# Kernel tuning notes

Hardware: AMD Instinct MI355X
Metric: run time of the kernel (lower is better)

## Reference

```python
import jax, jax.numpy as jnp
import numpy as np

B, L, DIN, DH, DE = 16, 128, 768, 300, 100
ALPHA = 0.2
NEG = -9e15


def setup_inputs() -> dict:
    key = jax.random.key(0)
    k = jax.random.split(key, 7)
    s = lambda fan: 1.0 / np.sqrt(fan)
    return {
        "x": jax.random.normal(k[0], (B, L, DIN), jnp.float32),
        "adj": jax.random.randint(k[1], (B, L, L), 0, 2, jnp.int32),
        "edge_embedding": jax.random.normal(k[2], (B, L, L, DE), jnp.float32),
        "W": jax.random.normal(k[3], (DIN, DH), jnp.float32) * s(DIN),
        "a": jax.random.normal(k[4], (2 * DH, 1), jnp.float32) * s(2 * DH),
        "edge_map_w": jax.random.normal(k[5], (DH, DE), jnp.float32) * s(DE),
        "edge_map_b": jnp.zeros((DH,), jnp.float32),
        "edge_lin_w": jax.random.normal(k[6], (1, DH), jnp.float32) * s(DH),
        "edge_lin_b": jnp.zeros((1,), jnp.float32),
    }


def _forward(x, edge_embedding, W, a, edge_map_w, edge_map_b, edge_lin_w, edge_lin_b, adj):
    h = x @ W  # [B, L, DH]
    # Faithful to torch: h.repeat_interleave(L, dim=2).view(B, L*L, DH) scrambles
    # features: a_input_first[b, i*L+j, d] = h[b, i, (j*DH + d) // L].
    # So e1[b,i,j] = sum_d h[b,i,(j*DH+d)//L] * a[d] = h[b,i] . V[j], with V[j,k] =
    # sum of a[d] over d where (j*DH+d)//L == k. Build V once by scatter-add.
    idx = (jnp.arange(L)[:, None] * DH + jnp.arange(DH)[None, :]) // L  # [L, DH], values in [0, DH)
    a_first = a[:DH, 0]
    V = jnp.zeros((L, DH), h.dtype).at[jnp.arange(L)[:, None], idx].add(a_first[None, :])  # [L, DH]
    e1 = jnp.einsum('bik,jk->bij', h, V)  # [B, L, L]
    # Second half: h.repeat_interleave(L, dim=0).view(...) gives plain h_j tiling.
    e2 = h @ a[DH:, 0]  # [B, L], broadcast over i
    e = jax.nn.leaky_relu(e1 + e2[:, None, :], ALPHA)  # [B, L, L]
    # Edge-weight gate (use_edge_weight == 'yes'); note torch relu result is discarded.
    em = edge_embedding @ edge_map_w.T + edge_map_b  # [B, L, L, DH]
    ew = jax.nn.sigmoid(em @ edge_lin_w.T + edge_lin_b)[..., 0]  # [B, L, L]
    e_final = e * ew
    att = jax.nn.softmax(jnp.where(adj > 0, e_final, NEG), axis=2)  # dropout off (eval)
    return h + jnp.matmul(att, h)  # residual add, concat=False


def reference(x, adj, edge_embedding, W, a, edge_map_w, edge_map_b, edge_lin_w, edge_lin_b):
    return _forward(x, edge_embedding, W, a, edge_map_w, edge_map_b, edge_lin_w, edge_lin_b, adj)
```

## Files before the change

kernel.cpp:

```cpp
#include <hip/hip_runtime.h>
#include <hip/hip_bf16.h>


#define L 128
#define DH 300
#define DIN 768
#define DE 100
#define SPLITK 4
#define MROWS 2048
#define SL ((size_t)MROWS * DH)

typedef __bf16 bf16x8 __attribute__((ext_vector_type(8)));
typedef float f32x4 __attribute__((ext_vector_type(4)));
typedef unsigned short ushort_t;

__device__ __forceinline__ ushort_t f2bf(float f) {
    __bf16 h = (__bf16)f;
    ushort_t u;
    __builtin_memcpy(&u, &h, 2);
    return u;
}

__global__ __launch_bounds__(256) void k_small(
    const float* __restrict__ A,
    const float* __restrict__ EMW,
    const float* __restrict__ EMB,
    const float* __restrict__ ELW,
    const float* __restrict__ ELB,
    float* __restrict__ CV, float* __restrict__ C0,
    float* __restrict__ VW, int* __restrict__ VCOL)
{
    int t = threadIdx.x;
    if (blockIdx.x == 0) {
        if (t < DE) {
            float s = 0.f;
            for (int k = 0; k < DH; ++k)
                s += ELW[k] * EMW[k * DE + t];
            CV[t] = s;
        } else if (t == DE) {
            float s = 0.f;
            for (int k = 0; k < DH; ++k)
                s += ELW[k] * EMB[k];
            C0[0] = s + ELB[0];
        }
    } else {
        if (t < L) {
            int base = t * DH;
            int cm = base >> 7;
            float w0 = 0.f, w1 = 0.f, w2 = 0.f, w3 = 0.f;
            for (int j = 0; j < DH; ++j) {
                int u = ((base + j) >> 7) - cm;
                float av = A[j];
                w0 += (u == 0) ? av : 0.f;
                w1 += (u == 1) ? av : 0.f;
                w2 += (u == 2) ? av : 0.f;
                w3 += (u == 3) ? av : 0.f;
            }
            VCOL[t] = cm;
            VW[t * 4 + 0] = w0; VW[t * 4 + 1] = w1;
            VW[t * 4 + 2] = w2; VW[t * 4 + 3] = w3;
        }
    }
}

__global__ __launch_bounds__(256) void k_cvt(
    const float* __restrict__ Wm, ushort_t* __restrict__ WT)
{
    __shared__ float tile[64][65];
    int k0 = blockIdx.x * 64;
    int c0 = blockIdx.y * 64;
    int t = threadIdx.x;
#pragma unroll
    for (int s = 0; s < 16; ++s) {
        int idx = t + 256 * s;
        int kr = idx >> 6, cc = idx & 63;
        int c = c0 + cc;
        tile[kr][cc] = (c < DH) ? Wm[(size_t)(k0 + kr) * DH + c] : 0.f;
    }
    __syncthreads();
#pragma unroll
    for (int s = 0; s < 16; ++s) {
        int idx = t + 256 * s;
        int c = idx >> 6, kr = idx & 63;
        WT[(size_t)(c0 + c) * DIN + k0 + kr] = f2bf(tile[kr][c]);
    }
}

__global__ __launch_bounds__(256) void k_gemm(
    const float* __restrict__ X,
    const ushort_t* __restrict__ WT,
    float* __restrict__ HP)
{
    __shared__ ushort_t As[64 * 72];
    __shared__ ushort_t Bs[64 * 72];
    int t = threadIdx.x;
    int w = t >> 6;
    int lane = t & 63;
    int lr = lane & 15;
    int lk = lane >> 4;
    int r0 = blockIdx.y * 64;
    int c0 = blockIdx.x * 64;
    int kbase = blockIdx.z * (DIN / SPLITK);

    f32x4 acc[4];
#pragma unroll
    for (int ct = 0; ct < 4; ++ct) acc[ct] = (f32x4){0.f, 0.f, 0.f, 0.f};

    int srow = t >> 2, skq = (t & 3) * 16;

    for (int step = 0; step < 3; ++step) {
        int kk = kbase + step * 64;
        {
            const float4* xs = (const float4*)(X + (size_t)(r0 + srow) * DIN + kk + skq);
            float4 f0 = xs[0], f1 = xs[1], f2 = xs[2], f3 = xs[3];
            bf16x8 v0, v1;
            v0[0] = (__bf16)f0.x; v0[1] = (__bf16)f0.y; v0[2] = (__bf16)f0.z; v0[3] = (__bf16)f0.w;
            v0[4] = (__bf16)f1.x; v0[5] = (__bf16)f1.y; v0[6] = (__bf16)f1.z; v0[7] = (__bf16)f1.w;
            v1[0] = (__bf16)f2.x; v1[1] = (__bf16)f2.y; v1[2] = (__bf16)f2.z; v1[3] = (__bf16)f2.w;
            v1[4] = (__bf16)f3.x; v1[5] = (__bf16)f3.y; v1[6] = (__bf16)f3.z; v1[7] = (__bf16)f3.w;
            *(bf16x8*)&As[srow * 72 + skq] = v0;
            *(bf16x8*)&As[srow * 72 + skq + 8] = v1;
        }
        {
            const uint4* wp = (const uint4*)(WT + (size_t)(c0 + srow) * DIN + kk + skq);
            uint4 u0 = wp[0], u1 = wp[1];
            *(uint4*)&Bs[srow * 72 + skq] = u0;
            *(uint4*)&Bs[srow * 72 + skq + 8] = u1;
        }
        __syncthreads();
#pragma unroll
        for (int k2 = 0; k2 < 2; ++k2) {
            bf16x8 af = *(bf16x8*)&As[(w * 16 + lr) * 72 + k2 * 32 + lk * 8];
#pragma unroll
            for (int ct = 0; ct < 4; ++ct) {
                bf16x8 bf_ = *(bf16x8*)&Bs[(ct * 16 + lr) * 72 + k2 * 32 + lk * 8];
                acc[ct] = __builtin_amdgcn_mfma_f32_16x16x32_bf16(af, bf_, acc[ct], 0, 0, 0);
            }
        }
        __syncthreads();
    }
    float* outp = HP + (size_t)blockIdx.z * SL;
#pragma unroll
    for (int ct = 0; ct < 4; ++ct) {
        int col = c0 + ct * 16 + lr;
        if (col < DH) {
#pragma unroll
            for (int r = 0; r < 4; ++r) {
                int row = r0 + w * 16 + lk * 4 + r;
                outp[(size_t)row * DH + col] = acc[ct][r];
            }
        }
    }
}

__global__ __launch_bounds__(256) void k_red(
    const float* __restrict__ HP, const float* __restrict__ A,
    float* __restrict__ H, float* __restrict__ E2)
{
    int t = threadIdx.x;
    int row = blockIdx.x * 8 + (t >> 5);
    int lane = t & 31;
    const float4* a4 = (const float4*)(A + DH);
    float4* hout = (float4*)(H + (size_t)row * DH);
    float acc = 0.f;
    for (int k4 = lane; k4 < DH / 4; k4 += 32) {
        float4 hv; hv.x = 0.f; hv.y = 0.f; hv.z = 0.f; hv.w = 0.f;
#pragma unroll
        for (int z = 0; z < SPLITK; ++z) {
            float4 v = ((const float4*)(HP + (size_t)z * SL + (size_t)row * DH))[k4];
            hv.x += v.x; hv.y += v.y; hv.z += v.z; hv.w += v.w;
        }
        float4 av = a4[k4];
        hout[k4] = hv;
        acc += hv.x * av.x + hv.y * av.y + hv.z * av.z + hv.w * av.w;
    }
#pragma unroll
    for (int o = 16; o >= 1; o >>= 1) acc += __shfl_xor(acc, o);
    if (lane == 0) E2[row] = acc;
}

__global__ __launch_bounds__(256) void k_attn(
    const float* __restrict__ EE,
    const int* __restrict__ ADJ,
    const float* __restrict__ H,
    const float* __restrict__ E2,
    const float* __restrict__ CV, const float* __restrict__ C0,
    const float* __restrict__ VW, const int* __restrict__ VCOL,
    float* __restrict__ OUT)
{
    __shared__ float eeb[32 * DE];
    __shared__ float hrow[DH];
    __shared__ float cl[DE];
    __shared__ float ef[L];
    __shared__ float att[L];
    __shared__ float red[4];

    int bid = blockIdx.x;
    int b = bid >> 7;
    int t = threadIdx.x;

    for (int k = t; k < DH; k += 256) hrow[k] = H[(size_t)bid * DH + k];
    if (t < DE) cl[t] = CV[t];

    int jg = t >> 3;
    int g  = t & 7;
    const float c0v = C0[0];

#pragma unroll
    for (int ch = 0; ch < 4; ++ch) {
        __syncthreads();
        const float4* src = (const float4*)(EE + (size_t)bid * (L * DE) + ch * 32 * DE);
        float4* dst = (float4*)eeb;
        for (int idx = t; idx < 800; idx += 256) dst[idx] = src[idx];
        __syncthreads();
        const float2* row = (const float2*)(eeb + jg * DE);
        const float2* cp = (const float2*)cl;
        float s = 0.f;
        for (int q = g; q < 50; q += 8) {
            float2 v = row[q], c2 = cp[q];
            s = fmaf(v.x, c2.x, fmaf(v.y, c2.y, s));
        }
        s += __shfl_xor(s, 1);
        s += __shfl_xor(s, 2);
        s += __shfl_xor(s, 4);
        if (g == 0) {
            int j = ch * 32 + jg;
            float ewv = 1.f / (1.f + expf(-(s + c0v)));
            int cm = VCOL[j];
            float e1 = 0.f;
#pragma unroll
            for (int u = 0; u < 4; ++u) {
                int c = cm + u; if (c > DH - 1) c = DH - 1;
                e1 += VW[j * 4 + u] * hrow[c];
            }
            float e = e1 + E2[(size_t)b * L + j];
            e = (e > 0.f) ? e : 0.2f * e;
            ef[j] = (ADJ[(size_t)bid * L + j] > 0) ? e * ewv : -9.0e15f;
        }
    }
    __syncthreads();

    float v = (t < L) ? ef[t] : -3.0e38f;
#pragma unroll
    for (int o = 32; o >= 1; o >>= 1) v = fmaxf(v, __shfl_xor(v, o));
    int wid = t >> 6;
    if ((t & 63) == 0) red[wid] = v;
    __syncthreads();
    float mx = fmaxf(fmaxf(red[0], red[1]), fmaxf(red[2], red[3]));
    __syncthreads();
    float p = (t < L) ? expf(ef[t] - mx) : 0.f;
    v = p;
#pragma unroll
    for (int o = 32; o >= 1; o >>= 1) v += __shfl_xor(v, o);
    if ((t & 63) == 0) red[wid] = v;
    __syncthreads();
    float denom = red[0] + red[1] + red[2] + red[3];
    if (t < L) att[t] = p / denom;
    __syncthreads();

    const float* Hb = H + (size_t)b * L * DH;
    for (int k = t; k < DH; k += 256) {
        float a0 = hrow[k], a1 = 0.f, a2 = 0.f, a3 = 0.f;
#pragma unroll 4
        for (int j = 0; j < L; j += 4) {
            a0 = fmaf(att[j + 0], Hb[(size_t)(j + 0) * DH + k], a0);
            a1 = fmaf(att[j + 1], Hb[(size_t)(j + 1) * DH + k], a1);
            a2 = fmaf(att[j + 2], Hb[(size_t)(j + 2) * DH + k], a2);
            a3 = fmaf(att[j + 3], Hb[(size_t)(j + 3) * DH + k], a3);
        }
        OUT[(size_t)bid * DH + k] = (a0 + a1) + (a2 + a3);
    }
}

extern "C" void kernel_launch(void* const* d_in, const int* in_sizes, int n_in,
                              void* d_out, int out_size, void* d_ws, size_t ws_size,
                              hipStream_t stream) {
    const float* X   = (const float*)d_in[0];
    const int*   ADJ = (const int*)d_in[1];
    const float* EE  = (const float*)d_in[2];
    const float* Wm  = (const float*)d_in[3];
    const float* A   = (const float*)d_in[4];
    const float* EMW = (const float*)d_in[5];
    const float* EMB = (const float*)d_in[6];
    const float* ELW = (const float*)d_in[7];
    const float* ELB = (const float*)d_in[8];
    float* OUT = (float*)d_out;

    float* ws = (float*)d_ws;
    float* HP   = ws;
    float* H    = ws + 2457600;
    float* E2   = ws + 3072000;
    float* CV   = ws + 3074048;
    float* C0   = ws + 3074148;
    float* VW   = ws + 3074152;
    int*   VCOL = (int*)(ws + 3074664);
    ushort_t* WT = (ushort_t*)(ws + 3074816);

    k_small<<<dim3(2), dim3(256), 0, stream>>>(A, EMW, EMB, ELW, ELB, CV, C0, VW, VCOL);
    k_cvt<<<dim3(12, 5), dim3(256), 0, stream>>>(Wm, WT);
    k_gemm<<<dim3(5, 32, SPLITK), dim3(256), 0, stream>>>(X, WT, HP);
    k_red<<<dim3(256), dim3(256), 0, stream>>>(HP, A, H, E2);
    k_attn<<<dim3(2048), dim3(256), 0, stream>>>(EE, ADJ, H, E2, CV, C0, VW, VCOL, OUT);
}
```

Baseline: 73.63 us.

## Split edge-gate dot into its own kernel and process two rows per softmax block

The fused attention kernel is split in two. k_ef streams the edge embeddings and writes the gate logits to a workspace buffer. k_sm_pv computes the scores, runs the softmax per wave, and does the att@H product for two query rows per block, so each load of H is shared by both rows. This targets the repeated H reads in the PV loop and lets the edge-streaming kernel run without depending on H or E2. The cost is an extra launch and a global round trip for S, and the second kernel has half as many blocks.

New measurement: 72.34 us. About the same (-1.7%).

```diff
diff --git a/kernel.cpp b/kernel.cpp
--- a/kernel.cpp
+++ b/kernel.cpp
@@ -8,6 +8,7 @@
 #define DE 100
 #define SPLITK 4
 #define MROWS 2048
+#define IG 2
 #define SL ((size_t)MROWS * DH)
 
 typedef __bf16 bf16x8 __attribute__((ext_vector_type(8)));
@@ -179,33 +180,18 @@
     if (lane == 0) E2[row] = acc;
 }
 
-__global__ __launch_bounds__(256) void k_attn(
-    const float* __restrict__ EE,
-    const int* __restrict__ ADJ,
-    const float* __restrict__ H,
-    const float* __restrict__ E2,
-    const float* __restrict__ CV, const float* __restrict__ C0,
-    const float* __restrict__ VW, const int* __restrict__ VCOL,
-    float* __restrict__ OUT)
+__global__ __launch_bounds__(256) void k_ef(
+    const float* __restrict__ EE, const float* __restrict__ CV,
+    const float* __restrict__ C0, float* __restrict__ S)
 {
     __shared__ float eeb[32 * DE];
-    __shared__ float hrow[DH];
     __shared__ float cl[DE];
-    __shared__ float ef[L];
-    __shared__ float att[L];
-    __shared__ float red[4];
-
     int bid = blockIdx.x;
-    int b = bid >> 7;
-    int t = threadIdx.x;
-
-    for (int k = t; k < DH; k += 256) hrow[k] = H[(size_t)bid * DH + k];
+    int t = threadIdx.x;
     if (t < DE) cl[t] = CV[t];
-
     int jg = t >> 3;
     int g  = t & 7;
     const float c0v = C0[0];
-
 #pragma unroll
     for (int ch = 0; ch < 4; ++ch) {
         __syncthreads();
@@ -223,52 +209,87 @@
         s += __shfl_xor(s, 1);
         s += __shfl_xor(s, 2);
         s += __shfl_xor(s, 4);
-        if (g == 0) {
-            int j = ch * 32 + jg;
-            float ewv = 1.f / (1.f + expf(-(s + c0v)));
-            int cm = VCOL[j];
-            float e1 = 0.f;
-#pragma unroll
-            for (int u = 0; u < 4; ++u) {
-                int c = cm + u; if (c > DH - 1) c = DH - 1;
-                e1 += VW[j * 4 + u] * hrow[c];
-            }
-            float e = e1 + E2[(size_t)b * L + j];
-            e = (e > 0.f) ? e : 0.2f * e;
-            ef[j] = (ADJ[(size_t)bid * L + j] > 0) ? e * ewv : -9.0e15f;
-        }
+        if (g == 0) S[(size_t)bid * L + ch * 32 + jg] = s + c0v;
+    }
+}
+
+__global__ __launch_bounds__(256) void k_sm_pv(
+    const float* __restrict__ S, const int* __restrict__ ADJ,
+    const float* __restrict__ H, const float* __restrict__ E2,
+    const float* __restrict__ VW, const int* __restrict__ VCOL,
+    float* __restrict__ OUT)
+{
+    __shared__ float hrow[IG][DH];
+    __shared__ float att[IG][L];
+    int blk = blockIdx.x;
+    int b = blk >> 6;
+    int i0 = (blk & 63) * IG;
+    int bid0 = b * L + i0;
+    int t = threadIdx.x;
+
+    for (int idx = t; idx < IG * DH; idx += 256) {
+        int r = idx / DH, k = idx - r * DH;
+        hrow[r][k] = H[(size_t)(bid0 + r) * DH + k];
     }
     __syncthreads();
 
-    float v = (t < L) ? ef[t] : -3.0e38f;
-#pragma unroll
-    for (int o = 32; o >= 1; o >>= 1) v = fmaxf(v, __shfl_xor(v, o));
-    int wid = t >> 6;
-    if ((t & 63) == 0) red[wid] = v;
+    {
+        int r = t >> 7, j = t & 127;
+        int bid = bid0 + r;
+        float s = S[(size_t)bid * L + j];
+        float ewv = 1.f / (1.f + expf(-s));
+        int cm = VCOL[j];
+        float e1 = 0.f;
+#pragma unroll
+        for (int u = 0; u < 4; ++u) {
+            int c = cm + u; if (c > DH - 1) c = DH - 1;
+            e1 += VW[j * 4 + u] * hrow[r][c];
+        }
+        float e = e1 + E2[(size_t)b * L + j];
+        e = (e > 0.f) ? e : 0.2f * e;
+        att[r][j] = (ADJ[(size_t)bid * L + j] > 0) ? e * ewv : -9.0e15f;
+    }
     __syncthreads();
-    float mx = fmaxf(fmaxf(red[0], red[1]), fmaxf(red[2], red[3]));
-    __syncthreads();
-    float p = (t < L) ? expf(ef[t] - mx) : 0.f;
-    v = p;
-#pragma unroll
-    for (int o = 32; o >= 1; o >>= 1) v += __shfl_xor(v, o);
-    if ((t & 63) == 0) red[wid] = v;
-    __syncthreads();
-    float denom = red[0] + red[1] + red[2] + red[3];
-    if (t < L) att[t] = p / denom;
+
+    {
+        int w = t >> 6, lane = t & 63;
+        if (w < IG) {
+            float v0 = att[w][lane], v1 = att[w][lane + 64];
+            float m = fmaxf(v0, v1);
+#pragma unroll
+            for (int o = 32; o >= 1; o >>= 1) m = fmaxf(m, __shfl_xor(m, o));
+            float p0 = expf(v0 - m), p1 = expf(v1 - m);
+            float sm = p0 + p1;
+#pragma unroll
+            for (int o = 32; o >= 1; o >>= 1) sm += __shfl_xor(sm, o);
+            float inv = 1.f / sm;
+            att[w][lane] = p0 * inv;
+            att[w][lane + 64] = p1 * inv;
+        }
+    }
     __syncthreads();
 
     const float* Hb = H + (size_t)b * L * DH;
     for (int k = t; k < DH; k += 256) {
-        float a0 = hrow[k], a1 = 0.f, a2 = 0.f, a3 = 0.f;
-#pragma unroll 4
+        float a0 = hrow[0][k], c0a = 0.f;
+        float a1 = hrow[1][k], c1a = 0.f;
+#pragma unroll 2
         for (int j = 0; j < L; j += 4) {
-            a0 = fmaf(att[j + 0], Hb[(size_t)(j + 0) * DH + k], a0);
-            a1 = fmaf(att[j + 1], Hb[(size_t)(j + 1) * DH + k], a1);
-            a2 = fmaf(att[j + 2], Hb[(size_t)(j + 2) * DH + k], a2);
-            a3 = fmaf(att[j + 3], Hb[(size_t)(j + 3) * DH + k], a3);
-        }
-        OUT[(size_t)bid * DH + k] = (a0 + a1) + (a2 + a3);
+            float h0 = Hb[(size_t)(j + 0) * DH + k];
+            float h1 = Hb[(size_t)(j + 1) * DH + k];
+            float h2 = Hb[(size_t)(j + 2) * DH + k];
+            float h3 = Hb[(size_t)(j + 3) * DH + k];
+            a0  = fmaf(att[0][j + 0], h0, a0);
+            c0a = fmaf(att[0][j + 1], h1, c0a);
+            a0  = fmaf(att[0][j + 2], h2, a0);
+            c0a = fmaf(att[0][j + 3], h3, c0a);
+            a1  = fmaf(att[1][j + 0], h0, a1);
+            c1a = fmaf(att[1][j + 1], h1, c1a);
+            a1  = fmaf(att[1][j + 2], h2, a1);
+            c1a = fmaf(att[1][j + 3], h3, c1a);
+        }
+        OUT[(size_t)(bid0 + 0) * DH + k] = a0 + c0a;
+        OUT[(size_t)(bid0 + 1) * DH + k] = a1 + c1a;
     }
 }
 
@@ -295,10 +316,12 @@
     float* VW   = ws + 3074152;
     int*   VCOL = (int*)(ws + 3074664);
     ushort_t* WT = (ushort_t*)(ws + 3074816);
+    float* Sbuf = ws + 3197696;
 
     k_small<<<dim3(2), dim3(256), 0, stream>>>(A, EMW, EMB, ELW, ELB, CV, C0, VW, VCOL);
     k_cvt<<<dim3(12, 5), dim3(256), 0, stream>>>(Wm, WT);
     k_gemm<<<dim3(5, 32, SPLITK), dim3(256), 0, stream>>>(X, WT, HP);
     k_red<<<dim3(256), dim3(256), 0, stream>>>(HP, A, H, E2);
-    k_attn<<<dim3(2048), dim3(256), 0, stream>>>(EE, ADJ, H, E2, CV, C0, VW, VCOL, OUT);
-}
+    k_ef<<<dim3(2048), dim3(256), 0, stream>>>(EE, CV, C0, Sbuf);
+    k_sm_pv<<<dim3(1024), dim3(256), 0, stream>>>(Sbuf, ADJ, H, E2, VW, VCOL, OUT);
+}
```
